# Kernel tuning notes

Hardware: AMD Instinct MI355X
Metric: run time of the kernel (lower is better)

The kernel has to match this reference:

```python
import jax, jax.numpy as jnp
import numpy as np

HIDDEN = 1024
NUM_HEADS = 16
HEAD_DIM = HIDDEN // NUM_HEADS
EPS = 1e-12


def _layernorm(x, g, b):
    mu = jnp.mean(x, axis=-1, keepdims=True)
    var = jnp.var(x, axis=-1, keepdims=True)
    return (x - mu) * jax.lax.rsqrt(var + EPS) * g + b


def _attention(q, k, v, mask, Wd, bd, ln_g, ln_b):
    # q: [B,T,H], k/v: [B,S,H], mask: [B,1,1,S] additive
    B, T, _ = q.shape
    S = k.shape[1]
    qh = q.reshape(B, T, NUM_HEADS, HEAD_DIM).transpose(0, 2, 1, 3)  # [B,h,T,d]
    kh = k.reshape(B, S, NUM_HEADS, HEAD_DIM).transpose(0, 2, 1, 3)
    vh = v.reshape(B, S, NUM_HEADS, HEAD_DIM).transpose(0, 2, 1, 3)
    scores = jnp.einsum('bhtd,bhsd->bhts', qh, kh) / jnp.sqrt(jnp.float32(HEAD_DIM))
    if mask is not None:
        scores = scores + mask
    probs = jax.nn.softmax(scores, axis=-1)  # dropout = identity in eval
    ctx = jnp.einsum('bhts,bhsd->bthd', probs, vh)  # [B,T,h,d]
    # torch: w = dense.weight.t().view(h, d, H); einsum('bfnd,ndh->bfh')
    w = Wd.T.reshape(NUM_HEADS, HEAD_DIM, HIDDEN)
    proj = jnp.einsum('bthd,hdH->btH', ctx, w) + bd
    # residual is the (projected) query tensor q, per source
    return _layernorm(q + proj, ln_g, ln_b)


def setup_inputs() -> dict:
    key = jax.random.key(0)
    ks = jax.random.split(key, 12)
    s = 0.02
    B, S, T = 4, 1024, 1024
    return {
        'encoder_states': jax.random.normal(ks[0], (B, S, HIDDEN), jnp.float32),
        'decoder_inputs': jax.random.normal(ks[1], (B, T, HIDDEN), jnp.float32),
        'src_attention_mask': jnp.zeros((B, 1, 1, S), jnp.float32),
        'tgt_attention_mask': jnp.zeros((B, 1, 1, T), jnp.float32),
        'Wq': jax.random.normal(ks[2], (HIDDEN, HIDDEN), jnp.float32) * s,
        'bq': jnp.zeros((HIDDEN,), jnp.float32),
        'Wk': jax.random.normal(ks[3], (HIDDEN, HIDDEN), jnp.float32) * s,
        'bk': jnp.zeros((HIDDEN,), jnp.float32),
        'Wv': jax.random.normal(ks[4], (HIDDEN, HIDDEN), jnp.float32) * s,
        'bv': jnp.zeros((HIDDEN,), jnp.float32),
        'Wd': jax.random.normal(ks[5], (HIDDEN, HIDDEN), jnp.float32) * s,
        'bd': jnp.zeros((HIDDEN,), jnp.float32),
        'ln_g': jnp.ones((HIDDEN,), jnp.float32),
        'ln_b': jnp.zeros((HIDDEN,), jnp.float32),
    }


def reference(encoder_states, decoder_inputs, src_attention_mask, tgt_attention_mask,
              Wq, bq, Wk, bk, Wv, bv, Wd, bd, ln_g, ln_b):
    # projections (torch Linear: x @ W.T + b)
    q1 = decoder_inputs @ Wq.T + bq
    k1 = decoder_inputs @ Wk.T + bk
    v1 = decoder_inputs @ Wv.T + bv
    ek = encoder_states @ Wk.T + bk
    ev = encoder_states @ Wv.T + bv
    # self-attention over decoder states
    self_out = _attention(q1, k1, v1, tgt_attention_mask, Wd, bd, ln_g, ln_b)
    # cross-attention: query = self_out directly (no extra projection, per source)
    out = _attention(self_out, ek, ev, src_attention_mask, Wd, bd, ln_g, ln_b)
    return out
```

## Files before the change

### kernel.cpp

```cpp
#include <hip/hip_runtime.h>
#include <stdint.h>


#define B_   4
#define T_   1024
#define S_   1024
#define H_   1024
#define LOG2E 1.44269504088896340736f
#define SCALE_K (0.125f * LOG2E)

typedef __attribute__((ext_vector_type(8)))  __bf16       bf16x8;
typedef __attribute__((ext_vector_type(4)))  float        f32x4;
typedef __attribute__((ext_vector_type(16))) float        f32x16;
typedef __attribute__((ext_vector_type(4)))  unsigned int uint4v;

static __device__ __forceinline__ float bf2f(unsigned int u) {
    return __builtin_bit_cast(float, u << 16);
}
static __device__ __forceinline__ unsigned short f2bf(float f) {
    unsigned int x = __builtin_bit_cast(unsigned int, f);
    return (unsigned short)((x + 0x7fffu + ((x >> 16) & 1u)) >> 16);
}
static __device__ __forceinline__ unsigned int cvt_pk_bf16(float lo, float hi) {
    unsigned int r;
    asm("v_cvt_pk_bf16_f32 %0, %1, %2" : "=v"(r) : "v"(lo), "v"(hi));
    return r;
}
static __device__ __forceinline__ void perm32swap(unsigned int& a, unsigned int& b) {
    asm("v_permlane32_swap_b32 %0, %1" : "+v"(a), "+v"(b));
}
static __device__ __forceinline__ f32x4 mfma16(bf16x8 a, bf16x8 b, f32x4 c) {
    return __builtin_amdgcn_mfma_f32_16x16x32_bf16(a, b, c, 0, 0, 0);
}
static __device__ __forceinline__ f32x16 mfma32(bf16x8 a, bf16x8 b, f32x16 c) {
    return __builtin_amdgcn_mfma_f32_32x32x16_bf16(a, b, c, 0, 0, 0);
}

typedef const __attribute__((address_space(1))) void gv_t;
typedef __attribute__((address_space(3))) void lv_t;
static __device__ __forceinline__ void g2lds16(const void* g, void* l) {
    __builtin_amdgcn_global_load_lds((gv_t*)(size_t)g, (lv_t*)(unsigned int)(size_t)l, 16, 0, 0);
}

struct CvtArgs {
    const float* src[6];
    unsigned short* dst[6];
    float scale[6];
    int n4[6];
};
__global__ __launch_bounds__(256)
void cvt_multi(CvtArgs a) {
    const int k = blockIdx.y;
    const int i = blockIdx.x * 256 + threadIdx.x;
    if (i >= a.n4[k]) return;
    const float s = a.scale[k];
    float4 v = ((const float4*)a.src[k])[i];
    uint2 o;
    o.x = (unsigned)f2bf(v.x * s) | ((unsigned)f2bf(v.y * s) << 16);
    o.y = (unsigned)f2bf(v.z * s) | ((unsigned)f2bf(v.w * s) << 16);
    ((uint2*)a.dst[k])[i] = o;
}

struct GemmJob {
    const unsigned short* A[5];
    const unsigned short* W[5];
    const float* bias[5];
    float bs[5];
    unsigned short* O[5];
};
__global__ __launch_bounds__(256, 2)
void gemm_bf16(GemmJob job)
{
    __shared__ char smem[32768];
    char* As = smem;
    char* Bs = smem + 16384;
    const int tid = threadIdx.x;
    const int lane = tid & 63;
    const int w = tid >> 6;
    const int c = lane & 15, g = lane >> 4;
    const int wm = (w >> 1) * 64, wn = (w & 1) * 64;
    const int m0 = blockIdx.x * 128;
    const int set = blockIdx.y >> 3;
    const int n0 = (blockIdx.y & 7) * 128;
    const unsigned short* A    = job.A[set];
    const unsigned short* W    = job.W[set];
    const float* bias          = job.bias[set];
    const float bscale         = job.bs[set];
    unsigned short* O          = job.O[set];

    f32x4 acc[4][4];
#pragma unroll
    for (int i = 0; i < 4; i++)
#pragma unroll
        for (int j = 0; j < 4; j++) acc[i][j] = (f32x4){0.f, 0.f, 0.f, 0.f};

    const int srow = w * 32 + (lane >> 3);
    const int swzc = ((lane & 7) ^ (lane >> 3)) * 8;
    const unsigned short* gA = A + (size_t)(m0 + srow) * 1024 + swzc;
    const unsigned short* gB = W + (size_t)(n0 + srow) * 1024 + swzc;
    char* lA = As + w * 4096;
    char* lB = Bs + w * 4096;

    for (int kk = 0; kk < 1024; kk += 64) {
#pragma unroll
        for (int q = 0; q < 4; q++) {
            g2lds16(gA + kk + q*8192, lA + q*1024);
            g2lds16(gB + kk + q*8192, lB + q*1024);
        }
        __syncthreads();
#pragma unroll
        for (int ksub = 0; ksub < 2; ksub++) {
            bf16x8 af[4], bfr[4];
#pragma unroll
            for (int t = 0; t < 4; t++) {
                const int ra = wm + t*16 + c;
                const int rb = wn + t*16 + c;
                const int so = ((ksub*4 + g) ^ (c & 7)) << 4;
                af[t]  = *(const bf16x8*)(As + ra*128 + so);
                bfr[t] = *(const bf16x8*)(Bs + rb*128 + so);
            }
#pragma unroll
            for (int i = 0; i < 4; i++)
#pragma unroll
                for (int j = 0; j < 4; j++)
                    acc[i][j] = mfma16(af[i], bfr[j], acc[i][j]);
        }
        __syncthreads();
    }

    float bvv[4];
#pragma unroll
    for (int j = 0; j < 4; j++) bvv[j] = bias[n0 + wn + j*16 + c] * bscale;
    char* eb = As + w * 4096;
#pragma unroll
    for (int p = 0; p < 2; p++) {
#pragma unroll
        for (int ii = 0; ii < 2; ii++) {
            const int i = p*2 + ii;
#pragma unroll
            for (int j = 0; j < 4; j++)
#pragma unroll
                for (int r = 0; r < 4; r++)
                    *(unsigned short*)(eb + (ii*16 + g*4 + r)*128 + (c + j*16)*2)
                        = f2bf(acc[i][j][r] + bvv[j]);
        }
        asm volatile("s_waitcnt lgkmcnt(0)" ::: "memory");
#pragma unroll
        for (int it = 0; it < 4; it++) {
            const int lrow = it*8 + (lane >> 3);
            uint4 vv = *(const uint4*)(eb + lrow*128 + (lane & 7)*16);
            *(uint4*)(O + (size_t)(m0 + wm + p*32 + lrow)*1024 + n0 + wn + (lane & 7)*8) = vv;
        }
        if (p == 0) asm volatile("s_waitcnt lgkmcnt(0)" ::: "memory");
    }
}

__global__ __launch_bounds__(256)
void transpose_v2(const unsigned short* __restrict__ V0, unsigned short* __restrict__ VT0,
                  const unsigned short* __restrict__ V1, unsigned short* __restrict__ VT1)
{
    __shared__ char sm[8192];
    const unsigned short* V = blockIdx.z ? V1 : V0;
    unsigned short* VT      = blockIdx.z ? VT1 : VT0;
    const int tid = threadIdx.x;
    const int bh = blockIdx.y, b = bh >> 4, h = bh & 15;
    const int s0 = blockIdx.x * 64;
    for (int u = tid; u < 512; u += 256) {
        const int r = u >> 3, sg = u & 7;
        uint4 v = *(const uint4*)(V + (size_t)(b*S_ + s0 + r)*H_ + h*64 + sg*8);
        *(uint4*)(sm + r*128 + ((sg*16) ^ ((r & 7) << 4))) = v;
    }
    __syncthreads();
    const int d = tid >> 2, ss = tid & 3;
    unsigned int ow[8];
#pragma unroll
    for (int j2 = 0; j2 < 8; j2++) {
        const int s_a = ss*16 + 2*j2, s_b = s_a + 1;
        unsigned int ta = *(const unsigned short*)(sm + s_a*128 + ((2*d) ^ ((s_a & 7) << 4)));
        unsigned int tb = *(const unsigned short*)(sm + s_b*128 + ((2*d) ^ ((s_b & 7) << 4)));
        ow[j2] = ta | (tb << 16);
    }
    unsigned short* op = VT + (size_t)(bh*64 + d)*S_ + s0 + ss*16;
    uint4 o0, o1;
    o0.x = ow[0]; o0.y = ow[1]; o0.z = ow[2]; o0.w = ow[3];
    o1.x = ow[4]; o1.y = ow[5]; o1.z = ow[6]; o1.w = ow[7];
    *(uint4*)op = o0;
    *(uint4*)(op + 8) = o1;
}

__global__ __launch_bounds__(256, 4)
void attn_fused3(const unsigned short* __restrict__ Q,
                 const unsigned short* __restrict__ Kx,
                 const unsigned short* __restrict__ VT,
                 const float* __restrict__ mask,
                 unsigned short* __restrict__ Octx)
{
    __shared__ char smem[32768 + 4096 + 16];
    float* mb = (float*)(smem + 32768);
    int* flag = (int*)(smem + 32768 + 4096);

    const int tid = threadIdx.x;
    const int lane = tid & 63, w = tid >> 6;
    const int qc = lane & 31, hi = lane >> 5;
    const int bh = blockIdx.y, b = bh >> 4, h = bh & 15;
    const int q0 = blockIdx.x * 128 + w * 32;

    const int rs = tid >> 3, sg = tid & 7;
    const int scol = (sg ^ (rs & 7)) * 8;
    const unsigned short* gK = Kx + (size_t)(b*S_ + rs)*H_ + h*64 + scol;
    const unsigned short* gV = VT + (size_t)(bh*64 + rs)*S_ + scol;
    char* ldK = smem + w * 1024;
    char* ldV = smem + 8192 + w * 1024;

    const unsigned short* qptr = Q + (size_t)(b*T_ + q0 + qc)*H_ + h*64 + hi*8;
    bf16x8 qf[4];
#pragma unroll
    for (int s = 0; s < 4; s++) qf[s] = *(const bf16x8*)(qptr + s*16);

    uint4v onesw;
    onesw[0] = 0x3f803f80u; onesw[1] = 0x3f803f80u; onesw[2] = 0x3f803f80u; onesw[3] = 0x3f803f80u;
    const bf16x8 ones = __builtin_bit_cast(bf16x8, onesw);

    if (tid == 0) *flag = 0;
    g2lds16(gK,           ldK);
    g2lds16(gK + 32*H_,   ldK + 4096);
    g2lds16(gV,           ldV);
    g2lds16(gV + 32*S_,   ldV + 4096);
    __syncthreads();
    {
        float4 mv = ((const float4*)(mask + (size_t)b*S_))[tid];
        float4 ms;
        ms.x = mv.x * LOG2E; ms.y = mv.y * LOG2E; ms.z = mv.z * LOG2E; ms.w = mv.w * LOG2E;
        ((float4*)mb)[tid] = ms;
        if (mv.x != 0.f || mv.y != 0.f || mv.z != 0.f || mv.w != 0.f) atomicOr(flag, 1);
    }
    __syncthreads();
    const int msk = *flag;

    f32x16 o0 = {}, o1 = {}, lsum = {};

    for (int t = 0; t < 16; ++t) {
        if (t < 15) {
            const int nb = (t + 1) & 1;
            const size_t ko = (size_t)(t + 1) * 64 * H_;
            const int    vo = (t + 1) * 64;
            g2lds16(gK + ko,          ldK + nb*16384);
            g2lds16(gK + ko + 32*H_,  ldK + nb*16384 + 4096);
            g2lds16(gV + vo,          ldV + nb*16384);
            g2lds16(gV + vo + 32*S_,  ldV + nb*16384 + 4096);
        }
        const char* Ks = smem + (t & 1) * 16384;
        const char* Vs = Ks + 8192;

        f32x16 st0 = {}, st1 = {};
        __builtin_amdgcn_s_setprio(1);
#pragma unroll
        for (int step = 0; step < 4; ++step) {
            bf16x8 ak = *(const bf16x8*)(Ks + qc*128 + ((step*32 + hi*16) ^ ((qc & 7) << 4)));
            st0 = mfma32(ak, qf[step], st0);
        }
#pragma unroll
        for (int step = 0; step < 4; ++step) {
            bf16x8 ak = *(const bf16x8*)(Ks + (32 + qc)*128 + ((step*32 + hi*16) ^ ((qc & 7) << 4)));
            st1 = mfma32(ak, qf[step], st1);
        }
        __builtin_amdgcn_s_setprio(0);

#pragma unroll
        for (int ts = 0; ts < 2; ++ts) {
            f32x16& st = ts ? st1 : st0;
            if (msk) {
#pragma unroll
                for (int rq = 0; rq < 4; ++rq) {
                    const float4 bb = *(const float4*)(mb + t*64 + ts*32 + rq*8 + hi*4);
#pragma unroll
                    for (int e = 0; e < 4; ++e)
                        st[rq*4 + e] = __builtin_amdgcn_exp2f(st[rq*4 + e] + (&bb.x)[e]);
                }
            } else {
#pragma unroll
                for (int r = 0; r < 16; ++r) st[r] = __builtin_amdgcn_exp2f(st[r]);
            }

#pragma unroll
            for (int half = 0; half < 2; ++half) {
                unsigned w0 = cvt_pk_bf16(st[half*8 + 0], st[half*8 + 1]);
                unsigned w1 = cvt_pk_bf16(st[half*8 + 2], st[half*8 + 3]);
                unsigned w2 = cvt_pk_bf16(st[half*8 + 4], st[half*8 + 5]);
                unsigned w3 = cvt_pk_bf16(st[half*8 + 6], st[half*8 + 7]);
                perm32swap(w0, w2);
                perm32swap(w1, w3);
                uint4v fw; fw[0] = w0; fw[1] = w1; fw[2] = w2; fw[3] = w3;
                const bf16x8 pa = __builtin_bit_cast(bf16x8, fw);
                const int vcol = (ts*64 + half*32 + hi*16) ^ ((qc & 7) << 4);
                bf16x8 v0 = *(const bf16x8*)(Vs + qc*128        + vcol);
                bf16x8 v1 = *(const bf16x8*)(Vs + (32 + qc)*128 + vcol);
                __builtin_amdgcn_s_setprio(1);
                o0   = mfma32(pa, v0,   o0);
                o1   = mfma32(pa, v1,   o1);
                lsum = mfma32(pa, ones, lsum);
                __builtin_amdgcn_s_setprio(0);
            }
        }
        __syncthreads();
    }

#pragma unroll
    for (int dt = 0; dt < 2; ++dt) {
        const f32x16& oo = dt ? o1 : o0;
#pragma unroll
        for (int r = 0; r < 16; ++r) {
            const int qrow = (r & 3) + 8*(r >> 2) + 4*hi;
            const float val = oo[r] / lsum[r];
            Octx[(size_t)(b*T_ + q0 + qrow)*H_ + h*64 + dt*32 + qc] = f2bf(val);
        }
    }
}

template<int OUTMODE>
__global__ __launch_bounds__(256)
void ln_kernel(const unsigned short* __restrict__ resid,
               const unsigned short* __restrict__ proj,
               const float* __restrict__ gam,
               const float* __restrict__ bet,
               unsigned short* __restrict__ obf,
               float* __restrict__ of32)
{
    __shared__ float red[8];
    const int tid = threadIdx.x;
    const int lane = tid & 63, w = tid >> 6;
    const int i = tid * 4;
    const size_t base = (size_t)blockIdx.x * 1024 + i;
    uint2 rv = *(const uint2*)(resid + base);
    uint2 pv = *(const uint2*)(proj + base);
    float x[4];
    x[0] = bf2f(rv.x & 0xffffu) + bf2f(pv.x & 0xffffu);
    x[1] = bf2f(rv.x >> 16)     + bf2f(pv.x >> 16);
    x[2] = bf2f(rv.y & 0xffffu) + bf2f(pv.y & 0xffffu);
    x[3] = bf2f(rv.y >> 16)     + bf2f(pv.y >> 16);
    float s = x[0] + x[1] + x[2] + x[3];
    float q = x[0]*x[0] + x[1]*x[1] + x[2]*x[2] + x[3]*x[3];
#pragma unroll
    for (int off = 1; off < 64; off <<= 1) {
        s += __shfl_xor(s, off);
        q += __shfl_xor(q, off);
    }
    if (lane == 0) { red[w*2] = s; red[w*2 + 1] = q; }
    __syncthreads();
    s = red[0] + red[2] + red[4] + red[6];
    q = red[1] + red[3] + red[5] + red[7];
    const float mu   = s * (1.f/1024.f);
    const float var  = q * (1.f/1024.f) - mu*mu;
    const float rstd = rsqrtf(var + 1e-12f);
    const float4 gv = *(const float4*)(gam + i);
    const float4 bv = *(const float4*)(bet + i);
    float y[4];
#pragma unroll
    for (int j = 0; j < 4; j++)
        y[j] = (x[j] - mu) * rstd * (&gv.x)[j] + (&bv.x)[j];
    if (OUTMODE == 0) {
        uint2 oo;
        oo.x = (unsigned)f2bf(y[0]) | ((unsigned)f2bf(y[1]) << 16);
        oo.y = (unsigned)f2bf(y[2]) | ((unsigned)f2bf(y[3]) << 16);
        *(uint2*)(obf + base) = oo;
    } else {
        float4 oo; oo.x = y[0]; oo.y = y[1]; oo.z = y[2]; oo.w = y[3];
        *(float4*)(of32 + base) = oo;
    }
}

extern "C" void kernel_launch(void* const* d_in, const int* in_sizes, int n_in,
                              void* d_out, int out_size, void* d_ws, size_t ws_size,
                              hipStream_t stream)
{
    const float* enc   = (const float*)d_in[0];
    const float* dec   = (const float*)d_in[1];
    const float* smask = (const float*)d_in[2];
    const float* tmask = (const float*)d_in[3];
    const float* Wq = (const float*)d_in[4];
    const float* bq = (const float*)d_in[5];
    const float* Wk = (const float*)d_in[6];
    const float* bk = (const float*)d_in[7];
    const float* Wv = (const float*)d_in[8];
    const float* bv = (const float*)d_in[9];
    const float* Wd = (const float*)d_in[10];
    const float* bd = (const float*)d_in[11];
    const float* lng = (const float*)d_in[12];
    const float* lnb = (const float*)d_in[13];
    float* out = (float*)d_out;

    char* ws = (char*)d_ws;
    const size_t MB = 1024ull * 1024ull;
    unsigned short* dec_bf = (unsigned short*)(ws + 0*MB);
    unsigned short* enc_bf = (unsigned short*)(ws + 8*MB);
    unsigned short* Wq_bf  = (unsigned short*)(ws + 16*MB);
    unsigned short* Wk_bf  = (unsigned short*)(ws + 18*MB);
    unsigned short* Wv_bf  = (unsigned short*)(ws + 20*MB);
    unsigned short* Wd_bf  = (unsigned short*)(ws + 22*MB);
    unsigned short* q1  = (unsigned short*)(ws + 24*MB);
    unsigned short* k1  = (unsigned short*)(ws + 32*MB);
    unsigned short* v1  = (unsigned short*)(ws + 40*MB);
    unsigned short* ek  = (unsigned short*)(ws + 48*MB);
    unsigned short* ev  = (unsigned short*)(ws + 56*MB);
    unsigned short* vt1 = (unsigned short*)(ws + 64*MB);
    unsigned short* ctx      = dec_bf;
    unsigned short* proj     = enc_bf;
    unsigned short* self_out = k1;
    unsigned short* evt      = v1;

    CvtArgs ca;
    ca.src[0] = dec; ca.dst[0] = dec_bf; ca.scale[0] = 1.f;      ca.n4[0] = 1048576;
    ca.src[1] = enc; ca.dst[1] = enc_bf; ca.scale[1] = 1.f;      ca.n4[1] = 1048576;
    ca.src[2] = Wq;  ca.dst[2] = Wq_bf;  ca.scale[2] = 1.f;      ca.n4[2] = 262144;
    ca.src[3] = Wk;  ca.dst[3] = Wk_bf;  ca.scale[3] = SCALE_K;  ca.n4[3] = 262144;
    ca.src[4] = Wv;  ca.dst[4] = Wv_bf;  ca.scale[4] = 1.f;      ca.n4[4] = 262144;
    ca.src[5] = Wd;  ca.dst[5] = Wd_bf;  ca.scale[5] = 1.f;      ca.n4[5] = 262144;
    cvt_multi<<<dim3(4096, 6), 256, 0, stream>>>(ca);

    GemmJob j1;
    j1.A[0] = dec_bf; j1.W[0] = Wq_bf; j1.bias[0] = bq; j1.bs[0] = 1.f;     j1.O[0] = q1;
    j1.A[1] = dec_bf; j1.W[1] = Wk_bf; j1.bias[1] = bk; j1.bs[1] = SCALE_K; j1.O[1] = k1;
    j1.A[2] = dec_bf; j1.W[2] = Wv_bf; j1.bias[2] = bv; j1.bs[2] = 1.f;     j1.O[2] = v1;
    j1.A[3] = enc_bf; j1.W[3] = Wk_bf; j1.bias[3] = bk; j1.bs[3] = SCALE_K; j1.O[3] = ek;
    j1.A[4] = enc_bf; j1.W[4] = Wv_bf; j1.bias[4] = bv; j1.bs[4] = 1.f;     j1.O[4] = ev;
    gemm_bf16<<<dim3(32, 40), 256, 0, stream>>>(j1);

    transpose_v2<<<dim3(16, 64, 2), 256, 0, stream>>>(v1, vt1, ev, evt);

    GemmJob jd;
    for (int i = 0; i < 5; i++) {
        jd.A[i] = ctx; jd.W[i] = Wd_bf; jd.bias[i] = bd; jd.bs[i] = 1.f; jd.O[i] = proj;
    }

    attn_fused3<<<dim3(8, 64), 256, 0, stream>>>(q1, k1, vt1, tmask, ctx);
    gemm_bf16<<<dim3(32, 8), 256, 0, stream>>>(jd);
    ln_kernel<0><<<4096, 256, 0, stream>>>(q1, proj, lng, lnb, self_out, nullptr);

    attn_fused3<<<dim3(8, 64), 256, 0, stream>>>(self_out, ek, evt, smask, ctx);
    gemm_bf16<<<dim3(32, 8), 256, 0, stream>>>(jd);
    ln_kernel<1><<<4096, 256, 0, stream>>>(self_out, proj, lng, lnb, nullptr, out);
}
```

Before: 183.1 us.

## Split KV sequence across two wave groups per attention block and reduce in LDS

Doubles the attention block to 512 threads, with two groups of four waves each processing half of the key/value sequence for the same query rows. Partial outputs and row sums are combined through shared memory before normalization, which is valid because the unnormalized exp sums are additive. This aims to raise wave occupancy and shorten the serial KV loop, at the cost of doubled LDS per block, an extra reduction and sync, and possible register pressure under the new launch bounds.

```diff
diff --git a/kernel.cpp b/kernel.cpp
--- a/kernel.cpp
+++ b/kernel.cpp
@@ -188,29 +188,32 @@
     *(uint4*)(op + 8) = o1;
 }
 
-__global__ __launch_bounds__(256, 4)
-void attn_fused3(const unsigned short* __restrict__ Q,
+__global__ __launch_bounds__(512, 4)
+void attn_fused4(const unsigned short* __restrict__ Q,
                  const unsigned short* __restrict__ Kx,
                  const unsigned short* __restrict__ VT,
                  const float* __restrict__ mask,
                  unsigned short* __restrict__ Octx)
 {
-    __shared__ char smem[32768 + 4096 + 16];
-    float* mb = (float*)(smem + 32768);
-    int* flag = (int*)(smem + 32768 + 4096);
+    __shared__ char smem[65536 + 4096 + 16];
+    float* mb = (float*)(smem + 65536);
+    int* flag = (int*)(smem + 65536 + 4096);
 
     const int tid = threadIdx.x;
     const int lane = tid & 63, w = tid >> 6;
+    const int wg = w & 3, shalf = w >> 2;
     const int qc = lane & 31, hi = lane >> 5;
     const int bh = blockIdx.y, b = bh >> 4, h = bh & 15;
-    const int q0 = blockIdx.x * 128 + w * 32;
-
-    const int rs = tid >> 3, sg = tid & 7;
+    const int q0 = blockIdx.x * 128 + wg * 32;
+
+    const int tg = wg * 64 + lane;
+    const int rs = tg >> 3, sg = tg & 7;
     const int scol = (sg ^ (rs & 7)) * 8;
-    const unsigned short* gK = Kx + (size_t)(b*S_ + rs)*H_ + h*64 + scol;
-    const unsigned short* gV = VT + (size_t)(bh*64 + rs)*S_ + scol;
-    char* ldK = smem + w * 1024;
-    char* ldV = smem + 8192 + w * 1024;
+    const unsigned short* gK = Kx + (size_t)(b*S_ + shalf*512 + rs)*H_ + h*64 + scol;
+    const unsigned short* gV = VT + (size_t)(bh*64 + rs)*S_ + shalf*512 + scol;
+    char* sbase = smem + shalf * 32768;
+    char* ldK = sbase + wg * 1024;
+    char* ldV = sbase + 8192 + wg * 1024;
 
     const unsigned short* qptr = Q + (size_t)(b*T_ + q0 + qc)*H_ + h*64 + hi*8;
     bf16x8 qf[4];
@@ -222,12 +225,12 @@
     const bf16x8 ones = __builtin_bit_cast(bf16x8, onesw);
 
     if (tid == 0) *flag = 0;
-    g2lds16(gK,           ldK);
-    g2lds16(gK + 32*H_,   ldK + 4096);
-    g2lds16(gV,           ldV);
-    g2lds16(gV + 32*S_,   ldV + 4096);
+    g2lds16(gK,          ldK);
+    g2lds16(gK + 32*H_,  ldK + 4096);
+    g2lds16(gV,          ldV);
+    g2lds16(gV + 32*S_,  ldV + 4096);
     __syncthreads();
-    {
+    if (tid < 256) {
         float4 mv = ((const float4*)(mask + (size_t)b*S_))[tid];
         float4 ms;
         ms.x = mv.x * LOG2E; ms.y = mv.y * LOG2E; ms.z = mv.z * LOG2E; ms.w = mv.w * LOG2E;
@@ -239,8 +242,8 @@
 
     f32x16 o0 = {}, o1 = {}, lsum = {};
 
-    for (int t = 0; t < 16; ++t) {
-        if (t < 15) {
+    for (int t = 0; t < 8; ++t) {
+        if (t < 7) {
             const int nb = (t + 1) & 1;
             const size_t ko = (size_t)(t + 1) * 64 * H_;
             const int    vo = (t + 1) * 64;
@@ -249,30 +252,25 @@
             g2lds16(gV + vo,          ldV + nb*16384);
             g2lds16(gV + vo + 32*S_,  ldV + nb*16384 + 4096);
         }
-        const char* Ks = smem + (t & 1) * 16384;
+        const char* Ks = sbase + (t & 1) * 16384;
         const char* Vs = Ks + 8192;
 
-        f32x16 st0 = {}, st1 = {};
-        __builtin_amdgcn_s_setprio(1);
-#pragma unroll
-        for (int step = 0; step < 4; ++step) {
-            bf16x8 ak = *(const bf16x8*)(Ks + qc*128 + ((step*32 + hi*16) ^ ((qc & 7) << 4)));
-            st0 = mfma32(ak, qf[step], st0);
-        }
-#pragma unroll
-        for (int step = 0; step < 4; ++step) {
-            bf16x8 ak = *(const bf16x8*)(Ks + (32 + qc)*128 + ((step*32 + hi*16) ^ ((qc & 7) << 4)));
-            st1 = mfma32(ak, qf[step], st1);
-        }
-        __builtin_amdgcn_s_setprio(0);
-
 #pragma unroll
         for (int ts = 0; ts < 2; ++ts) {
-            f32x16& st = ts ? st1 : st0;
+            f32x16 st = {};
+            __builtin_amdgcn_s_setprio(1);
+#pragma unroll
+            for (int step = 0; step < 4; ++step) {
+                bf16x8 ak = *(const bf16x8*)(Ks + (ts*32 + qc)*128 +
+                             ((step*32 + hi*16) ^ ((qc & 7) << 4)));
+                st = mfma32(ak, qf[step], st);
+            }
+            __builtin_amdgcn_s_setprio(0);
+
             if (msk) {
 #pragma unroll
                 for (int rq = 0; rq < 4; ++rq) {
-                    const float4 bb = *(const float4*)(mb + t*64 + ts*32 + rq*8 + hi*4);
+                    const float4 bb = *(const float4*)(mb + shalf*512 + t*64 + ts*32 + rq*8 + hi*4);
 #pragma unroll
                     for (int e = 0; e < 4; ++e)
                         st[rq*4 + e] = __builtin_amdgcn_exp2f(st[rq*4 + e] + (&bb.x)[e]);
@@ -305,14 +303,34 @@
         __syncthreads();
     }
 
-#pragma unroll
-    for (int dt = 0; dt < 2; ++dt) {
-        const f32x16& oo = dt ? o1 : o0;
+    float* cb = (float*)smem;
+    if (shalf == 1) {
+        float* dst = cb + wg*3072 + lane*48;
 #pragma unroll
         for (int r = 0; r < 16; ++r) {
-            const int qrow = (r & 3) + 8*(r >> 2) + 4*hi;
-            const float val = oo[r] / lsum[r];
-            Octx[(size_t)(b*T_ + q0 + qrow)*H_ + h*64 + dt*32 + qc] = f2bf(val);
+            dst[r]      = o0[r];
+            dst[16 + r] = o1[r];
+            dst[32 + r] = lsum[r];
+        }
+    }
+    __syncthreads();
+    if (shalf == 0) {
+        const float* src = cb + wg*3072 + lane*48;
+#pragma unroll
+        for (int r = 0; r < 16; ++r) {
+            o0[r]   += src[r];
+            o1[r]   += src[16 + r];
+            lsum[r] += src[32 + r];
+        }
+#pragma unroll
+        for (int dt = 0; dt < 2; ++dt) {
+            const f32x16& oo = dt ? o1 : o0;
+#pragma unroll
+            for (int r = 0; r < 16; ++r) {
+                const int qrow = (r & 3) + 8*(r >> 2) + 4*hi;
+                const float val = oo[r] / lsum[r];
+                Octx[(size_t)(b*T_ + q0 + qrow)*H_ + h*64 + dt*32 + qc] = f2bf(val);
+            }
         }
     }
 }
@@ -432,11 +450,11 @@
         jd.A[i] = ctx; jd.W[i] = Wd_bf; jd.bias[i] = bd; jd.bs[i] = 1.f; jd.O[i] = proj;
     }
 
-    attn_fused3<<<dim3(8, 64), 256, 0, stream>>>(q1, k1, vt1, tmask, ctx);
+    attn_fused4<<<dim3(8, 64), 512, 0, stream>>>(q1, k1, vt1, tmask, ctx);
     gemm_bf16<<<dim3(32, 8), 256, 0, stream>>>(jd);
     ln_kernel<0><<<4096, 256, 0, stream>>>(q1, proj, lng, lnb, self_out, nullptr);
 
-    attn_fused3<<<dim3(8, 64), 256, 0, stream>>>(self_out, ek, evt, smask, ctx);
+    attn_fused4<<<dim3(8, 64), 512, 0, stream>>>(self_out, ek, evt, smask, ctx);
     gemm_bf16<<<dim3(32, 8), 256, 0, stream>>>(jd);
     ln_kernel<1><<<4096, 256, 0, stream>>>(self_out, proj, lng, lnb, nullptr, out);
 }
```

Result: no change. 183.4 us (+0.1%).
